# Optimization experiments

Measured on AMD Instinct MI355X. Metric: run time of the kernel, lower is better.

## Reference

```python
import jax, jax.numpy as jnp
import numpy as np

B, S, T = 64, 128, 16
VOCAB, ENT_VOCAB = 50000, 400000
E_ELMO, D_TRI = 1024, 100


def setup_inputs() -> dict:
    key = jax.random.key(0)
    k1, k2, k3, k4, k5 = jax.random.split(key, 5)
    inputs = jax.random.randint(k1, (B, S), 0, VOCAB, dtype=jnp.int64 if jax.config.jax_enable_x64 else jnp.int32)
    triples = jax.random.randint(k2, (B, S, T, 3), 0, ENT_VOCAB, dtype=jnp.int32)
    id2_ids_batch = jax.random.randint(k3, (B, S, T), 0, 3, dtype=jnp.int32)
    embedding_table = jax.random.normal(k4, (VOCAB, E_ELMO), dtype=jnp.float32)
    entity_table = jax.random.normal(k5, (ENT_VOCAB, D_TRI), dtype=jnp.float32)
    return {
        "inputs": inputs,
        "triples": triples,
        "id2_ids_batch": id2_ids_batch,
        "embedding_table": embedding_table,
        "entity_table": entity_table,
    }


def reference(inputs, triples, id2_ids_batch, embedding_table, entity_table):
    """Vocabulary-level triple fusion (add_triples=True hot path).

    For each token (i,k): over triple slots j, flag==1 gathers the tail entity
    embedding (triples[...,1]), flag==2 gathers the head (triples[...,0]);
    others are skipped. Valid gathers are averaged; the token embedding part
    cancels (summed a times, divided by a). Result t = concat(tok_emb, avg),
    with zeros in the triple part when no valid triple exists.
    """
    tok = embedding_table[inputs]                      # [B,S,E]
    m1 = id2_ids_batch == 1                            # use tail entity
    m2 = id2_ids_batch == 2                            # use head entity
    valid = m1 | m2                                    # [B,S,T]
    ent_idx = jnp.where(m1, triples[..., 1], triples[..., 0])  # [B,S,T]
    gathered = entity_table[ent_idx] * valid[..., None].astype(entity_table.dtype)  # [B,S,T,D]
    cnt = valid.sum(axis=-1)                           # [B,S]
    denom = jnp.maximum(cnt, 1).astype(entity_table.dtype)[..., None]
    avg = gathered.sum(axis=-2) / denom                # [B,S,D]
    avg = jnp.where((cnt > 0)[..., None], avg, jnp.zeros((), dtype=avg.dtype))
    return jnp.concatenate([tok, avg], axis=-1)        # [B,S,E+D]
```

## Files before the change

### kernel.cpp

```cpp
#include <hip/hip_runtime.h>

constexpr int Bc = 64;
constexpr int Sc = 128;
constexpr int Tc = 16;
constexpr int Ec = 1024;
constexpr int Dc = 100;
constexpr int OUTD = Ec + Dc;

__global__ __launch_bounds__(256) void triple_fuse_kernel(
    const int*   __restrict__ inputs,
    const int*   __restrict__ triples,
    const int*   __restrict__ id2,
    const float* __restrict__ emb,
    const float* __restrict__ ent,
    float*       __restrict__ out)
{
    const int token = blockIdx.x;
    const int tid   = threadIdx.x;

    __shared__ int s_idx[Tc];

    if (tid < Tc) {
        const int slot = token * Tc + tid;
        const int flag = id2[slot];
        const int tri0 = triples[slot * 3 + 0];
        const int tri1 = triples[slot * 3 + 1];
        int e = -1;
        if (flag == 1) e = tri1;
        else if (flag == 2) e = tri0;
        s_idx[tid] = e;
    }
    __syncthreads();

    const long trow = (long)inputs[token] * Ec;
    const float4 v = ((const float4*)(emb + trow))[tid];
    ((float4*)(out + (long)token * OUTD))[tid] = v;

    if (tid < Dc) {
        float sum = 0.f;
        int   cnt = 0;
        #pragma unroll
        for (int j = 0; j < Tc; ++j) {
            const int e = s_idx[j];
            if (e >= 0) {
                sum += ent[(long)e * Dc + tid];
                ++cnt;
            }
        }
        const float avg = (cnt > 0) ? sum / (float)cnt : 0.f;
        out[(long)token * OUTD + Ec + tid] = avg;
    }
}

extern "C" void kernel_launch(void* const* d_in, const int* in_sizes, int n_in,
                              void* d_out, int out_size, void* d_ws, size_t ws_size,
                              hipStream_t stream) {
    const int*   inputs  = (const int*)d_in[0];
    const int*   triples = (const int*)d_in[1];
    const int*   id2     = (const int*)d_in[2];
    const float* emb     = (const float*)d_in[3];
    const float* ent     = (const float*)d_in[4];
    float*       out     = (float*)d_out;

    const int n_tokens = Bc * Sc;
    triple_fuse_kernel<<<n_tokens, 256, 0, stream>>>(inputs, triples, id2, emb, ent, out);
}
```

Measured before the change: 340.9 us.

## Compact valid triple indices via ballot and stage entity rows in shared memory

Issues the token-embedding load before the index setup. Compacts the valid entity indices with a wavefront ballot and popcount, so only valid slots are visited. Loads all valid entity rows in parallel with float4 across all 256 threads into shared memory, instead of 100 threads each issuing 16 serial dependent scalar loads. The goal is more memory-level parallelism for the random entity gathers, at the cost of about 6.4KB of LDS per block and an extra barrier.

```diff
diff --git a/kernel.cpp b/kernel.cpp
--- a/kernel.cpp
+++ b/kernel.cpp
@@ -18,37 +18,46 @@
     const int token = blockIdx.x;
     const int tid   = threadIdx.x;
 
-    __shared__ int s_idx[Tc];
+    __shared__ int   s_idx[Tc];
+    __shared__ int   s_cnt;
+    __shared__ float s_g[Tc * Dc];
 
+    const long trow = (long)inputs[token] * Ec;
+    const float4 tv = ((const float4*)(emb + trow))[tid];
+
+    int e = -1;
     if (tid < Tc) {
         const int slot = token * Tc + tid;
         const int flag = id2[slot];
-        const int tri0 = triples[slot * 3 + 0];
-        const int tri1 = triples[slot * 3 + 1];
-        int e = -1;
-        if (flag == 1) e = tri1;
-        else if (flag == 2) e = tri0;
-        s_idx[tid] = e;
+        if (flag == 1)      e = triples[slot * 3 + 1];
+        else if (flag == 2) e = triples[slot * 3 + 0];
+    }
+    if (tid < 64) {
+        const unsigned long long m = __ballot(e >= 0);
+        if (e >= 0) {
+            const int pos = __popcll(m & ((1ull << tid) - 1ull));
+            s_idx[pos] = e;
+        }
+        if (tid == 0) s_cnt = (int)__popcll(m);
+    }
+    __syncthreads();
+    const int cnt = s_cnt;
+
+    ((float4*)(out + (long)token * OUTD))[tid] = tv;
+
+    const int total = cnt * 25;
+    for (int i = tid; i < total; i += 256) {
+        const int j = i / 25;
+        const int p = i - j * 25;
+        const float4 g = ((const float4*)(ent + (long)s_idx[j] * Dc))[p];
+        ((float4*)s_g)[i] = g;
     }
     __syncthreads();
 
-    const long trow = (long)inputs[token] * Ec;
-    const float4 v = ((const float4*)(emb + trow))[tid];
-    ((float4*)(out + (long)token * OUTD))[tid] = v;
-
     if (tid < Dc) {
         float sum = 0.f;
-        int   cnt = 0;
-        #pragma unroll
-        for (int j = 0; j < Tc; ++j) {
-            const int e = s_idx[j];
-            if (e >= 0) {
-                sum += ent[(long)e * Dc + tid];
-                ++cnt;
-            }
-        }
-        const float avg = (cnt > 0) ? sum / (float)cnt : 0.f;
-        out[(long)token * OUTD + Ec + tid] = avg;
+        for (int j = 0; j < cnt; ++j) sum += s_g[j * Dc + tid];
+        out[(long)token * OUTD + Ec + tid] = (cnt > 0) ? sum / (float)cnt : 0.f;
     }
 }
 
@@ -62,6 +71,5 @@
     const float* ent     = (const float*)d_in[4];
     float*       out     = (float*)d_out;
 
-    const int n_tokens = Bc * Sc;
-    triple_fuse_kernel<<<n_tokens, 256, 0, stream>>>(inputs, triples, id2, emb, ent, out);
+    triple_fuse_kernel<<<Bc * Sc, 256, 0, stream>>>(inputs, triples, id2, emb, ent, out);
 }
```

Measured after the change: 331.3 us. 1.03x faster.
